# Kernel optimization log

Measured on AMD Instinct MI355X. Metric: run time of the kernel, lower is better.

The kernel has to match this reference:

```python
import jax, jax.numpy as jnp
import numpy as np

N = 100000   # nodes per type (author == paper count here)
E = 800000   # edges per edge type
D = 128      # input feature dim
HID = 128    # hidden_channels
OUT = 64     # out_channels
L = 2        # num_layers


def setup_inputs() -> dict:
    key = jax.random.key(0)
    ks = jax.random.split(key, 14)
    x_author = jax.random.normal(ks[0], (N, D), jnp.float32)
    x_paper = jax.random.normal(ks[1], (N, D), jnp.float32)
    edge_ap = jnp.stack([
        jax.random.randint(ks[2], (E,), 0, N),
        jax.random.randint(ks[3], (E,), 0, N),
    ]).astype(jnp.int32)  # [2,E] author->paper (src,dst)
    # paper->author: ensure every paper id appears as a source so the
    # meta-path conversion keeps all E edges (static shape under jit)
    pa_src = jnp.concatenate([jnp.arange(N), jax.random.randint(ks[4], (E - N,), 0, N)]).astype(jnp.int32)
    pa_dst = jax.random.randint(ks[5], (E,), 0, N).astype(jnp.int32)
    edge_pa = jnp.stack([pa_src, pa_dst])
    perm = jax.random.permutation(ks[6], N).astype(jnp.int32)  # DGI corruption
    s = 0.05
    # SAGEConv params: [layer, edge_type] with edge_type 0 = (author->paper), 1 = (paper->author)
    sage_Wl = jax.random.normal(ks[7], (L, 2, HID, D), jnp.float32) * s   # neighbor lin
    sage_Wr = jax.random.normal(ks[8], (L, 2, HID, D), jnp.float32) * s   # root lin
    sage_b = jnp.zeros((L, 2, HID), jnp.float32)
    # GATConv (heads=1) params
    gat_W = jax.random.normal(ks[9], (OUT, HID), jnp.float32) * s
    gat_att_src = jax.random.normal(ks[10], (OUT,), jnp.float32) * s
    gat_att_dst = jax.random.normal(ks[11], (OUT,), jnp.float32) * s
    gat_b = jnp.zeros((OUT,), jnp.float32)
    prelu_a = jnp.asarray(0.25, jnp.float32)
    return dict(x_author=x_author, x_paper=x_paper, sage_Wl=sage_Wl, sage_Wr=sage_Wr,
                sage_b=sage_b, gat_W=gat_W, gat_att_src=gat_att_src, gat_att_dst=gat_att_dst,
                gat_b=gat_b, prelu_a=prelu_a, edge_ap=edge_ap, edge_pa=edge_pa, perm=perm)


def _sage(x_src, x_dst, src, dst, Wl, Wr, b, n_dst):
    # SAGEConv: mean-aggregate neighbor feats, lin_l(agg) + lin_r(root) + bias
    agg = jax.ops.segment_sum(x_src[src], dst, num_segments=n_dst)       # [n_dst, D]
    cnt = jax.ops.segment_sum(jnp.ones((src.shape[0],), x_src.dtype), dst, num_segments=n_dst)
    mean = agg / jnp.maximum(cnt, 1.0)[:, None]
    return mean @ Wl.T + x_dst @ Wr.T + b


def _gat_prelu(feat, src, dst, W, a_src, a_dst, b, prelu_a, n):
    # GATConv heads=1 (self loops already appended by caller) + PReLU
    h = feat @ W.T                                                        # [n, OUT]
    e = jax.nn.leaky_relu((h @ a_src)[src] + (h @ a_dst)[dst], 0.2)       # [E']
    m = jax.ops.segment_max(e, dst, num_segments=n)
    ex = jnp.exp(e - m[dst])
    den = jax.ops.segment_sum(ex, dst, num_segments=n)
    coef = ex / den[dst]
    out = jax.ops.segment_sum(coef[:, None] * h[src], dst, num_segments=n) + b
    return jnp.where(out >= 0, out, prelu_a * out)


def reference(x_author, x_paper, sage_Wl, sage_Wr, sage_b, gat_W, gat_att_src,
              gat_att_dst, gat_b, prelu_a, edge_ap, edge_pa, perm):
    # Original loop feeds xx_dict into every layer, so only the LAST layer's
    # output survives; and only x_dict['author'] is consumed downstream.
    l = L - 1
    h_author = jax.nn.leaky_relu(
        _sage(x_paper, x_author, edge_pa[0], edge_pa[1],
              sage_Wl[l, 1], sage_Wr[l, 1], sage_b[l, 1], N), 0.01)
    # meta-path author->author edges (paper mapped via last-write paper->author dict)
    p2a = jnp.zeros((N,), jnp.int32).at[edge_pa[0]].set(edge_pa[1])
    self_loop = jnp.arange(N, dtype=jnp.int32)  # GATConv add_self_loops=True
    meta_src = jnp.concatenate([edge_ap[0], self_loop])
    meta_dst = jnp.concatenate([p2a[edge_ap[1]], self_loop])
    pos = _gat_prelu(h_author, meta_src, meta_dst, gat_W, gat_att_src, gat_att_dst, gat_b, prelu_a, N)
    neg = _gat_prelu(h_author[perm], meta_src, meta_dst, gat_W, gat_att_src, gat_att_dst, gat_b, prelu_a, N)
    summary = jnp.mean(pos, axis=0)
    return pos, neg, summary
```

## Files before the change

### kernel.cpp

```cpp
#include <hip/hip_runtime.h>
#include <stdint.h>

#define NN 100000
#define EE 800000
#define DD 128
#define HH 128
#define OO 64

#define SPA 40
#define SME 112

#define PREP_EDGE_B  391
#define PREP_CASTX_B 12500
#define PREP_CASTW_B 40
#define P2_SAGE_B    25000
#define P2_CMP_B     391
#define P3_GEMM_B    782
#define P3_META_B    391

typedef __attribute__((ext_vector_type(8))) short short8v;
typedef __attribute__((ext_vector_type(4))) float f32x4;

__device__ __forceinline__ unsigned short f2bf(float f) {
    union { float f; unsigned int u; } v; v.f = f;
    unsigned int u = v.u;
    u = (u + 0x7fffu + ((u >> 16) & 1u)) >> 16;
    return (unsigned short)u;
}
__device__ __forceinline__ float bf2f(unsigned short b) {
    union { unsigned int u; float f; } v; v.u = ((unsigned int)b) << 16;
    return v.f;
}

__global__ __launch_bounds__(256) void k_prep(const int* __restrict__ pa_src,
                                              const int* __restrict__ pa_dst,
                                              const float* __restrict__ x,
                                              const float* __restrict__ Wl,
                                              const float* __restrict__ Wr,
                                              const float* __restrict__ Wg,
                                              int* __restrict__ amax,
                                              int* __restrict__ cnt_pa,
                                              int* __restrict__ col_pa,
                                              unsigned short* __restrict__ xbf,
                                              unsigned short* __restrict__ wbf) {
    int b = blockIdx.x, t = threadIdx.x;
    if (b < PREP_EDGE_B) {
        int base = (b * 256 + t) * 8;
        if (base + 7 < EE) {
            int4 s0 = *(const int4*)(pa_src + base);
            int4 s1 = *(const int4*)(pa_src + base + 4);
            int4 d0 = *(const int4*)(pa_dst + base);
            int4 d1 = *(const int4*)(pa_dst + base + 4);
            int ss[8] = {s0.x, s0.y, s0.z, s0.w, s1.x, s1.y, s1.z, s1.w};
            int dd[8] = {d0.x, d0.y, d0.z, d0.w, d1.x, d1.y, d1.z, d1.w};
            int pos[8];
            #pragma unroll
            for (int k = 0; k < 8; ++k) atomicMax(&amax[ss[k]], base + k);
            #pragma unroll
            for (int k = 0; k < 8; ++k) pos[k] = atomicAdd(&cnt_pa[dd[k]], 1);
            #pragma unroll
            for (int k = 0; k < 8; ++k)
                if (pos[k] < SPA) __builtin_nontemporal_store(ss[k], &col_pa[dd[k] * SPA + pos[k]]);
        } else {
            for (int e = base; e < EE; ++e) {
                int s = pa_src[e], d = pa_dst[e];
                atomicMax(&amax[s], e);
                int pos = atomicAdd(&cnt_pa[d], 1);
                if (pos < SPA) __builtin_nontemporal_store(s, &col_pa[d * SPA + pos]);
            }
        }
    } else if (b < PREP_EDGE_B + PREP_CASTX_B) {
        long i = (long)(b - PREP_EDGE_B) * 256 + t;
        if (i >= (long)NN * DD / 4) return;
        float4 v = ((const float4*)x)[i];
        ushort4 w;
        w.x = f2bf(v.x); w.y = f2bf(v.y); w.z = f2bf(v.z); w.w = f2bf(v.w);
        ((ushort4*)xbf)[i] = w;
    } else {
        int i4 = (b - PREP_EDGE_B - PREP_CASTX_B) * 256 + t;
        if (i4 >= 10240) return;
        float4 v;
        if (i4 < 4096)       v = ((const float4*)Wl)[i4];
        else if (i4 < 8192)  v = ((const float4*)Wr)[i4 - 4096];
        else                 v = ((const float4*)Wg)[i4 - 8192];
        ushort4 w;
        w.x = f2bf(v.x); w.y = f2bf(v.y); w.z = f2bf(v.z); w.w = f2bf(v.w);
        ((ushort4*)wbf)[i4] = w;
    }
}

__global__ __launch_bounds__(256) void k_pack2(const int* __restrict__ cnt_pa,
                                               const int* __restrict__ col_pa,
                                               const unsigned short* __restrict__ xbf,
                                               const int* __restrict__ amax,
                                               const int* __restrict__ pa_dst,
                                               int* __restrict__ p2a32,
                                               unsigned short* __restrict__ mean_bf) {
    int b = blockIdx.x, t = threadIdx.x;
    if (b < P2_SAGE_B) {
        long gid = (long)b * 256 + t;
        int d = (int)(gid >> 6);
        if (d >= NN) return;
        int lane = (int)(gid & 63);
        int dcnt = cnt_pa[d];
        int deg = (dcnt > SPA) ? SPA : dcnt;
        const int* row = col_pa + d * SPA;
        float ax = 0.f, ay = 0.f;
        int i = 0;
        for (; i + 3 < deg; i += 4) {
            int s0 = row[i], s1 = row[i + 1], s2 = row[i + 2], s3 = row[i + 3];
            ushort2 v0 = ((const ushort2*)(xbf + (long)s0 * DD))[lane];
            ushort2 v1 = ((const ushort2*)(xbf + (long)s1 * DD))[lane];
            ushort2 v2 = ((const ushort2*)(xbf + (long)s2 * DD))[lane];
            ushort2 v3 = ((const ushort2*)(xbf + (long)s3 * DD))[lane];
            ax += (bf2f(v0.x) + bf2f(v1.x)) + (bf2f(v2.x) + bf2f(v3.x));
            ay += (bf2f(v0.y) + bf2f(v1.y)) + (bf2f(v2.y) + bf2f(v3.y));
        }
        for (; i < deg; ++i) {
            int s = row[i];
            ushort2 v = ((const ushort2*)(xbf + (long)s * DD))[lane];
            ax += bf2f(v.x);
            ay += bf2f(v.y);
        }
        float sc = 1.0f / fmaxf((float)dcnt, 1.0f);
        ushort2 w;
        w.x = f2bf(ax * sc);
        w.y = f2bf(ay * sc);
        ((ushort2*)(mean_bf + (long)d * DD))[lane] = w;
    } else {
        int s = (b - P2_SAGE_B) * 256 + t;
        if (s >= NN) return;
        p2a32[s] = pa_dst[amax[s]];
    }
}

__global__ __launch_bounds__(256) void k_pack3(const unsigned short* __restrict__ mean_bf,
                                               const float* __restrict__ xa,
                                               const unsigned short* __restrict__ wbf,
                                               const float* __restrict__ sb,
                                               const float* __restrict__ asrc,
                                               const float* __restrict__ adst,
                                               unsigned short* __restrict__ hg,
                                               float* __restrict__ al_s,
                                               float* __restrict__ al_d,
                                               const int* __restrict__ ap_src,
                                               const int* __restrict__ ap_dst,
                                               const int* __restrict__ p2a32,
                                               int* __restrict__ cnt_meta,
                                               int* __restrict__ col_meta) {
    __shared__ unsigned short hs[4 * 32 * 128];
    int b = blockIdx.x, t = threadIdx.x;
    if (b >= P3_GEMM_B) {
        int base = ((b - P3_GEMM_B) * 256 + t) * 8;
        if (base + 7 < EE) {
            int4 s0 = *(const int4*)(ap_src + base);
            int4 s1 = *(const int4*)(ap_src + base + 4);
            int4 t0 = *(const int4*)(ap_dst + base);
            int4 t1 = *(const int4*)(ap_dst + base + 4);
            int ss[8] = {s0.x, s0.y, s0.z, s0.w, s1.x, s1.y, s1.z, s1.w};
            int tt[8] = {t0.x, t0.y, t0.z, t0.w, t1.x, t1.y, t1.z, t1.w};
            int dd[8], pos[8];
            #pragma unroll
            for (int k = 0; k < 8; ++k) dd[k] = p2a32[tt[k]];
            #pragma unroll
            for (int k = 0; k < 8; ++k) pos[k] = atomicAdd(&cnt_meta[dd[k]], 1);
            #pragma unroll
            for (int k = 0; k < 8; ++k)
                if (pos[k] < SME) __builtin_nontemporal_store(ss[k], &col_meta[dd[k] * SME + pos[k]]);
        } else {
            for (int e = base; e < EE; ++e) {
                int d = p2a32[ap_dst[e]];
                int pos = atomicAdd(&cnt_meta[d], 1);
                if (pos < SME) __builtin_nontemporal_store(ap_src[e], &col_meta[d * SME + pos]);
            }
        }
        return;
    }
    const unsigned short* wl = wbf;
    const unsigned short* wr = wbf + 16384;
    const unsigned short* wg = wbf + 32768;
    int wave = t >> 6, lane = t & 63;
    int rowbase = b * 128 + wave * 32;
    int lr = lane & 15;
    int q = lane >> 4;
    int kq = q * 8;
    int r0 = rowbase + lr, r1 = r0 + 16;
    int cr0 = (r0 < NN) ? r0 : 0;
    int cr1 = (r1 < NN) ? r1 : 0;

    f32x4 acc[2][8];
    #pragma unroll
    for (int i = 0; i < 2; ++i)
        #pragma unroll
        for (int j = 0; j < 8; ++j) { f32x4 z = {0.f,0.f,0.f,0.f}; acc[i][j] = z; }

    #pragma unroll
    for (int k0 = 0; k0 < DD; k0 += 32) {
        int kk = k0 + kq;
        short8v am0 = *(const short8v*)(mean_bf + (long)cr0 * DD + kk);
        short8v am1 = *(const short8v*)(mean_bf + (long)cr1 * DD + kk);
        const float4* q0 = (const float4*)(xa + (long)cr0 * DD + kk);
        const float4* q1 = (const float4*)(xa + (long)cr1 * DD + kk);
        float4 a0 = q0[0], b0 = q0[1], a1 = q1[0], b1 = q1[1];
        short8v ax0, ax1;
        ax0[0]=(short)f2bf(a0.x); ax0[1]=(short)f2bf(a0.y); ax0[2]=(short)f2bf(a0.z); ax0[3]=(short)f2bf(a0.w);
        ax0[4]=(short)f2bf(b0.x); ax0[5]=(short)f2bf(b0.y); ax0[6]=(short)f2bf(b0.z); ax0[7]=(short)f2bf(b0.w);
        ax1[0]=(short)f2bf(a1.x); ax1[1]=(short)f2bf(a1.y); ax1[2]=(short)f2bf(a1.z); ax1[3]=(short)f2bf(a1.w);
        ax1[4]=(short)f2bf(b1.x); ax1[5]=(short)f2bf(b1.y); ax1[6]=(short)f2bf(b1.z); ax1[7]=(short)f2bf(b1.w);
        #pragma unroll
        for (int nb = 0; nb < 8; ++nb) {
            int o = nb * 16 + lr;
            short8v bl = *(const short8v*)(wl + o * DD + kk);
            short8v br = *(const short8v*)(wr + o * DD + kk);
            acc[0][nb] = __builtin_amdgcn_mfma_f32_16x16x32_bf16(am0, bl, acc[0][nb], 0, 0, 0);
            acc[1][nb] = __builtin_amdgcn_mfma_f32_16x16x32_bf16(am1, bl, acc[1][nb], 0, 0, 0);
            acc[0][nb] = __builtin_amdgcn_mfma_f32_16x16x32_bf16(ax0, br, acc[0][nb], 0, 0, 0);
            acc[1][nb] = __builtin_amdgcn_mfma_f32_16x16x32_bf16(ax1, br, acc[1][nb], 0, 0, 0);
        }
    }
    char* hbase = (char*)hs + wave * 8192;
    #pragma unroll
    for (int rh = 0; rh < 2; ++rh) {
        #pragma unroll
        for (int nb = 0; nb < 8; ++nb) {
            int col = nb * 16 + lr;
            float bias = sb[col];
            #pragma unroll
            for (int r = 0; r < 4; ++r) {
                int lrow = rh * 16 + q * 4 + r;
                float v = acc[rh][nb][r] + bias;
                v = (v >= 0.f) ? v : 0.01f * v;
                int boff = (lrow * 256 + col * 2) ^ ((lrow & 7) << 4);
                *(unsigned short*)(hbase + boff) = f2bf(v);
            }
        }
    }
    f32x4 acc2[2][4];
    #pragma unroll
    for (int i = 0; i < 2; ++i)
        #pragma unroll
        for (int j = 0; j < 4; ++j) { f32x4 z = {0.f,0.f,0.f,0.f}; acc2[i][j] = z; }

    #pragma unroll
    for (int k0 = 0; k0 < HH; k0 += 32) {
        int kk = k0 + kq;
        int boff0 = (lr * 256 + kk * 2) ^ ((lr & 7) << 4);
        int boff1 = ((16 + lr) * 256 + kk * 2) ^ ((lr & 7) << 4);
        short8v a0 = *(const short8v*)(hbase + boff0);
        short8v a1 = *(const short8v*)(hbase + boff1);
        #pragma unroll
        for (int nb = 0; nb < 4; ++nb) {
            short8v bg = *(const short8v*)(wg + (nb * 16 + lr) * HH + kk);
            acc2[0][nb] = __builtin_amdgcn_mfma_f32_16x16x32_bf16(a0, bg, acc2[0][nb], 0, 0, 0);
            acc2[1][nb] = __builtin_amdgcn_mfma_f32_16x16x32_bf16(a1, bg, acc2[1][nb], 0, 0, 0);
        }
    }
    float a_s[4], a_d[4];
    #pragma unroll
    for (int nb = 0; nb < 4; ++nb) { a_s[nb] = asrc[nb * 16 + lr]; a_d[nb] = adst[nb * 16 + lr]; }
    #pragma unroll
    for (int rh = 0; rh < 2; ++rh) {
        float ss[4] = {0.f,0.f,0.f,0.f}, dd[4] = {0.f,0.f,0.f,0.f};
        #pragma unroll
        for (int nb = 0; nb < 4; ++nb) {
            #pragma unroll
            for (int r = 0; r < 4; ++r) {
                int row = rowbase + rh * 16 + q * 4 + r;
                unsigned short wb = f2bf(acc2[rh][nb][r]);
                if (row < NN) hg[(long)row * OO + nb * 16 + lr] = wb;
                float w = bf2f(wb);
                ss[r] += w * a_s[nb];
                dd[r] += w * a_d[nb];
            }
        }
        #pragma unroll
        for (int r = 0; r < 4; ++r) {
            float s = ss[r], dv = dd[r];
            #pragma unroll
            for (int off = 1; off < 16; off <<= 1) {
                s  += __shfl_xor(s,  off, 64);
                dv += __shfl_xor(dv, off, 64);
            }
            int row = rowbase + rh * 16 + q * 4 + r;
            if (lr == 0 && row < NN) { al_s[row] = s; al_d[row] = dv; }
        }
    }
}

__global__ __launch_bounds__(256) void k_gat_gather(const int* __restrict__ cnt_meta,
                                                    const int* __restrict__ col_meta,
                                                    const int* __restrict__ perm,
                                                    const float* __restrict__ al_s,
                                                    const float* __restrict__ al_d,
                                                    const unsigned short* __restrict__ hg,
                                                    const float* __restrict__ gb,
                                                    const float* __restrict__ prelu_a,
                                                    float* __restrict__ out) {
    long gid = (long)blockIdx.x * 256 + threadIdx.x;
    int d = (int)(gid >> 6);
    if (d >= NN) return;
    int j = (int)(gid & 63);
    int deg = cnt_meta[d];
    if (deg > SME) deg = SME;
    const int* row = col_meta + d * SME;
    int pd = perm[d];
    float add = al_d[d];
    float adn = al_d[pd];
    float lp = al_s[d] + add;   lp = (lp >= 0.f) ? lp : 0.2f * lp;
    float ln = al_s[pd] + adn;  ln = (ln >= 0.f) ? ln : 0.2f * ln;
    float xps = __expf(lp), xns = __expf(ln);
    float denp = xps, denn = xns;
    float accp = xps * bf2f(hg[((long)d << 6) + j]);
    float accn = xns * bf2f(hg[((long)pd << 6) + j]);

    for (int base = 0; base < deg; base += 64) {
        int cnt = deg - base;
        if (cnt > 64) cnt = 64;
        int s = 0, ps = 0;
        float xp = 0.f, xn = 0.f;
        if (j < cnt) {
            s = row[base + j];
            ps = perm[s];
            float l0 = al_s[s] + add;   l0 = (l0 >= 0.f) ? l0 : 0.2f * l0;
            xp = __expf(l0);
            float m0 = al_s[ps] + adn;  m0 = (m0 >= 0.f) ? m0 : 0.2f * m0;
            xn = __expf(m0);
        }
        float tp = xp, tn = xn;
        #pragma unroll
        for (int off = 32; off; off >>= 1) {
            tp += __shfl_xor(tp, off, 64);
            tn += __shfl_xor(tn, off, 64);
        }
        denp += tp;
        denn += tn;
        int e = 0;
        for (; e + 3 < cnt; e += 4) {
            int s0 = __shfl(s, e),   s1 = __shfl(s, e + 1),   s2 = __shfl(s, e + 2),   s3 = __shfl(s, e + 3);
            int p0 = __shfl(ps, e),  p1 = __shfl(ps, e + 1),  p2 = __shfl(ps, e + 2),  p3 = __shfl(ps, e + 3);
            float a0 = __shfl(xp, e), a1 = __shfl(xp, e + 1), a2 = __shfl(xp, e + 2), a3 = __shfl(xp, e + 3);
            float b0 = __shfl(xn, e), b1 = __shfl(xn, e + 1), b2 = __shfl(xn, e + 2), b3 = __shfl(xn, e + 3);
            float h0 = bf2f(hg[((long)s0 << 6) + j]);
            float h1 = bf2f(hg[((long)s1 << 6) + j]);
            float h2 = bf2f(hg[((long)s2 << 6) + j]);
            float h3 = bf2f(hg[((long)s3 << 6) + j]);
            float g0 = bf2f(hg[((long)p0 << 6) + j]);
            float g1 = bf2f(hg[((long)p1 << 6) + j]);
            float g2 = bf2f(hg[((long)p2 << 6) + j]);
            float g3 = bf2f(hg[((long)p3 << 6) + j]);
            accp += (a0 * h0 + a1 * h1) + (a2 * h2 + a3 * h3);
            accn += (b0 * g0 + b1 * g1) + (b2 * g2 + b3 * g3);
        }
        for (; e < cnt; ++e) {
            int sb2 = __shfl(s, e);
            int pb = __shfl(ps, e);
            float ab = __shfl(xp, e);
            float bb = __shfl(xn, e);
            accp += ab * bf2f(hg[((long)sb2 << 6) + j]);
            accn += bb * bf2f(hg[((long)pb << 6) + j]);
        }
    }
    float bias = gb[j];
    float a = prelu_a[0];
    float vp = accp / denp + bias;
    vp = (vp >= 0.f) ? vp : a * vp;
    out[((long)d << 6) + j] = vp;
    float vn = accn / denn + bias;
    vn = (vn >= 0.f) ? vn : a * vn;
    out[((long)(NN + d) << 6) + j] = vn;
}

__global__ __launch_bounds__(256) void k_summary(const float* __restrict__ out_pos,
                                                 float* __restrict__ summary) {
    int t = threadIdx.x;
    int j = t & 63, sub = t >> 6;
    float acc = 0.f;
    for (int row = blockIdx.x * 4 + sub; row < NN; row += 256 * 4) {
        acc += out_pos[(long)row * OO + j];
    }
    __shared__ float red[4][OO];
    red[sub][j] = acc;
    __syncthreads();
    if (sub == 0) {
        float ttl = red[0][j] + red[1][j] + red[2][j] + red[3][j];
        atomicAdd(summary + j, ttl * (1.0f / NN));
    }
}

extern "C" void kernel_launch(void* const* d_in, const int* in_sizes, int n_in,
                              void* d_out, int out_size, void* d_ws, size_t ws_size,
                              hipStream_t stream) {
    const float* x_author = (const float*)d_in[0];
    const float* x_paper  = (const float*)d_in[1];
    const float* sage_Wl  = (const float*)d_in[2];
    const float* sage_Wr  = (const float*)d_in[3];
    const float* sage_b   = (const float*)d_in[4];
    const float* gat_W    = (const float*)d_in[5];
    const float* gat_as   = (const float*)d_in[6];
    const float* gat_ad   = (const float*)d_in[7];
    const float* gat_b    = (const float*)d_in[8];
    const float* prelu_a  = (const float*)d_in[9];
    const int*   edge_ap  = (const int*)d_in[10];
    const int*   edge_pa  = (const int*)d_in[11];
    const int*   perm     = (const int*)d_in[12];

    char* ws = (char*)d_ws;
    int*   cnt_pa    = (int*)(ws + 0);
    int*   cnt_meta  = (int*)(ws + 400000);
    int*   amax      = (int*)(ws + 800000);
    int*   p2a32     = (int*)(ws + 1200000);
    float* al_s      = (float*)(ws + 1600000);
    float* al_d      = (float*)(ws + 2000000);
    unsigned short* wbf = (unsigned short*)(ws + 2400000);
    int*   col_pa    = (int*)(ws + 2481920);
    unsigned short* mean_bf = (unsigned short*)(ws + 18481920);
    unsigned short* xbf     = (unsigned short*)(ws + 44081920);
    int*   col_meta  = (int*)(ws + 44081920);
    unsigned short* hg = (unsigned short*)col_pa;

    hipMemsetAsync(d_ws, 0, 1200000, stream);
    hipMemsetAsync((char*)d_out + (size_t)2 * NN * OO * sizeof(float), 0,
                   OO * sizeof(float), stream);

    const float* Wl = sage_Wl + 3 * HH * DD;
    const float* Wr = sage_Wr + 3 * HH * DD;
    const float* sb = sage_b  + 3 * HH;

    k_prep<<<PREP_EDGE_B + PREP_CASTX_B + PREP_CASTW_B, 256, 0, stream>>>(
        edge_pa, edge_pa + EE, x_paper, Wl, Wr, gat_W, amax, cnt_pa, col_pa, xbf, wbf);
    k_pack2<<<P2_SAGE_B + P2_CMP_B, 256, 0, stream>>>(
        cnt_pa, col_pa, xbf, amax, edge_pa + EE, p2a32, mean_bf);
    k_pack3<<<P3_GEMM_B + P3_META_B, 256, 0, stream>>>(
        mean_bf, x_author, wbf, sb, gat_as, gat_ad, hg, al_s, al_d,
        edge_ap, edge_ap + EE, p2a32, cnt_meta, col_meta);
    k_gat_gather<<<(NN * 64 + 255) / 256, 256, 0, stream>>>(cnt_meta, col_meta, perm,
                                                            al_s, al_d, hg, gat_b, prelu_a,
                                                            (float*)d_out);
    k_summary<<<256, 256, 0, stream>>>((float*)d_out, (float*)d_out + 2L * NN * OO);
}
```

Before: 337.2 us.

## Bucket edges by destination block then build CSR rows in shared memory

Replaces direct per-node atomic scatter into global adjacency rows with a two-pass scheme. Edges are first bucketed into 1024 coarse buckets of 98 destination nodes (packed local-dst<<17|src); per-bucket blocks then build fixed-width adjacency rows in LDS and write them out coalesced. This applies to both the SAGE paper->author graph and the meta-path graph, and also folds the p2a lookup into the meta scatter. It aims to cut scattered global atomics and random writes, at the cost of an extra kernel launch, extra passes over the edge data, and fixed bucket capacities that could silently drop edges on skewed inputs.

```diff
diff --git a/kernel.cpp b/kernel.cpp
--- a/kernel.cpp
+++ b/kernel.cpp
@@ -9,14 +9,17 @@
 
 #define SPA 40
 #define SME 112
+#define NB  1024
+#define BA  98
+#define CAPA 1024
+#define CAPM 2048
 
 #define PREP_EDGE_B  391
 #define PREP_CASTX_B 12500
 #define PREP_CASTW_B 40
-#define P2_SAGE_B    25000
-#define P2_CMP_B     391
-#define P3_GEMM_B    782
-#define P3_META_B    391
+#define SCATM_B      391
+#define SAGE_B       25000
+#define GEMM_B       782
 
 typedef __attribute__((ext_vector_type(8))) short short8v;
 typedef __attribute__((ext_vector_type(4))) float f32x4;
@@ -39,8 +42,8 @@
                                               const float* __restrict__ Wr,
                                               const float* __restrict__ Wg,
                                               int* __restrict__ amax,
-                                              int* __restrict__ cnt_pa,
-                                              int* __restrict__ col_pa,
+                                              int* __restrict__ curA,
+                                              int* __restrict__ sortedA,
                                               unsigned short* __restrict__ xbf,
                                               unsigned short* __restrict__ wbf) {
     int b = blockIdx.x, t = threadIdx.x;
@@ -53,20 +56,25 @@
             int4 d1 = *(const int4*)(pa_dst + base + 4);
             int ss[8] = {s0.x, s0.y, s0.z, s0.w, s1.x, s1.y, s1.z, s1.w};
             int dd[8] = {d0.x, d0.y, d0.z, d0.w, d1.x, d1.y, d1.z, d1.w};
-            int pos[8];
             #pragma unroll
             for (int k = 0; k < 8; ++k) atomicMax(&amax[ss[k]], base + k);
             #pragma unroll
-            for (int k = 0; k < 8; ++k) pos[k] = atomicAdd(&cnt_pa[dd[k]], 1);
-            #pragma unroll
-            for (int k = 0; k < 8; ++k)
-                if (pos[k] < SPA) __builtin_nontemporal_store(ss[k], &col_pa[dd[k] * SPA + pos[k]]);
+            for (int k = 0; k < 8; ++k) {
+                int bk = dd[k] / BA;
+                int pos = atomicAdd(&curA[bk], 1);
+                if (pos < CAPA)
+                    __builtin_nontemporal_store(((dd[k] - bk * BA) << 17) | ss[k],
+                                                &sortedA[bk * CAPA + pos]);
+            }
         } else {
             for (int e = base; e < EE; ++e) {
                 int s = pa_src[e], d = pa_dst[e];
                 atomicMax(&amax[s], e);
-                int pos = atomicAdd(&cnt_pa[d], 1);
-                if (pos < SPA) __builtin_nontemporal_store(s, &col_pa[d * SPA + pos]);
+                int bk = d / BA;
+                int pos = atomicAdd(&curA[bk], 1);
+                if (pos < CAPA)
+                    __builtin_nontemporal_store(((d - bk * BA) << 17) | s,
+                                                &sortedA[bk * CAPA + pos]);
             }
         }
     } else if (b < PREP_EDGE_B + PREP_CASTX_B) {
@@ -89,52 +97,93 @@
     }
 }
 
-__global__ __launch_bounds__(256) void k_pack2(const int* __restrict__ cnt_pa,
-                                               const int* __restrict__ col_pa,
-                                               const unsigned short* __restrict__ xbf,
+__global__ __launch_bounds__(256) void k_pack2(const int* __restrict__ ap_src,
+                                               const int* __restrict__ ap_dst,
                                                const int* __restrict__ amax,
                                                const int* __restrict__ pa_dst,
-                                               int* __restrict__ p2a32,
-                                               unsigned short* __restrict__ mean_bf) {
+                                               int* __restrict__ curM,
+                                               int* __restrict__ sortedM,
+                                               const int* __restrict__ curA,
+                                               const int* __restrict__ sortedA,
+                                               int* __restrict__ cnt_pa,
+                                               int* __restrict__ col_pa) {
+    __shared__ int cntA[BA];
+    __shared__ int colA[BA * SPA];
     int b = blockIdx.x, t = threadIdx.x;
-    if (b < P2_SAGE_B) {
-        long gid = (long)b * 256 + t;
-        int d = (int)(gid >> 6);
-        if (d >= NN) return;
-        int lane = (int)(gid & 63);
-        int dcnt = cnt_pa[d];
-        int deg = (dcnt > SPA) ? SPA : dcnt;
-        const int* row = col_pa + d * SPA;
-        float ax = 0.f, ay = 0.f;
-        int i = 0;
-        for (; i + 3 < deg; i += 4) {
-            int s0 = row[i], s1 = row[i + 1], s2 = row[i + 2], s3 = row[i + 3];
-            ushort2 v0 = ((const ushort2*)(xbf + (long)s0 * DD))[lane];
-            ushort2 v1 = ((const ushort2*)(xbf + (long)s1 * DD))[lane];
-            ushort2 v2 = ((const ushort2*)(xbf + (long)s2 * DD))[lane];
-            ushort2 v3 = ((const ushort2*)(xbf + (long)s3 * DD))[lane];
-            ax += (bf2f(v0.x) + bf2f(v1.x)) + (bf2f(v2.x) + bf2f(v3.x));
-            ay += (bf2f(v0.y) + bf2f(v1.y)) + (bf2f(v2.y) + bf2f(v3.y));
-        }
-        for (; i < deg; ++i) {
-            int s = row[i];
-            ushort2 v = ((const ushort2*)(xbf + (long)s * DD))[lane];
-            ax += bf2f(v.x);
-            ay += bf2f(v.y);
-        }
-        float sc = 1.0f / fmaxf((float)dcnt, 1.0f);
-        ushort2 w;
-        w.x = f2bf(ax * sc);
-        w.y = f2bf(ay * sc);
-        ((ushort2*)(mean_bf + (long)d * DD))[lane] = w;
-    } else {
-        int s = (b - P2_SAGE_B) * 256 + t;
-        if (s >= NN) return;
-        p2a32[s] = pa_dst[amax[s]];
-    }
-}
-
-__global__ __launch_bounds__(256) void k_pack3(const unsigned short* __restrict__ mean_bf,
+    if (b < SCATM_B) {
+        int base = (b * 256 + t) * 8;
+        #pragma unroll
+        for (int k = 0; k < 8; ++k) {
+            int e = base + k;
+            if (e < EE) {
+                int p = ap_dst[e];
+                int d = pa_dst[amax[p]];
+                int bk = d / BA;
+                int pos = atomicAdd(&curM[bk], 1);
+                if (pos < CAPM)
+                    __builtin_nontemporal_store(((d - bk * BA) << 17) | ap_src[e],
+                                                &sortedM[bk * CAPM + pos]);
+            }
+        }
+        return;
+    }
+    int bk = b - SCATM_B;
+    if (t < BA) cntA[t] = 0;
+    __syncthreads();
+    int n = curA[bk];
+    if (n > CAPA) n = CAPA;
+    const int* src = sortedA + bk * CAPA;
+    for (int i = t; i < n; i += 256) {
+        int w = src[i];
+        int dl = w >> 17, s = w & 0x1ffff;
+        int pos = atomicAdd(&cntA[dl], 1);
+        if (pos < SPA) colA[dl * SPA + pos] = s;
+    }
+    __syncthreads();
+    long gbase = (long)bk * BA;
+    if (t < BA && gbase + t < NN) cnt_pa[gbase + t] = cntA[t];
+    long cbase = gbase * SPA;
+    for (int i = t; i < BA * SPA; i += 256) {
+        if (gbase + i / SPA < NN) col_pa[cbase + i] = colA[i];
+    }
+}
+
+__global__ __launch_bounds__(256) void k_sage(const int* __restrict__ cnt_pa,
+                                              const int* __restrict__ col_pa,
+                                              const unsigned short* __restrict__ xbf,
+                                              unsigned short* __restrict__ mean_bf) {
+    long gid = (long)blockIdx.x * 256 + threadIdx.x;
+    int d = (int)(gid >> 6);
+    if (d >= NN) return;
+    int lane = (int)(gid & 63);
+    int dcnt = cnt_pa[d];
+    int deg = (dcnt > SPA) ? SPA : dcnt;
+    const int* row = col_pa + d * SPA;
+    float ax = 0.f, ay = 0.f;
+    int i = 0;
+    for (; i + 3 < deg; i += 4) {
+        int s0 = row[i], s1 = row[i + 1], s2 = row[i + 2], s3 = row[i + 3];
+        ushort2 v0 = ((const ushort2*)(xbf + (long)s0 * DD))[lane];
+        ushort2 v1 = ((const ushort2*)(xbf + (long)s1 * DD))[lane];
+        ushort2 v2 = ((const ushort2*)(xbf + (long)s2 * DD))[lane];
+        ushort2 v3 = ((const ushort2*)(xbf + (long)s3 * DD))[lane];
+        ax += (bf2f(v0.x) + bf2f(v1.x)) + (bf2f(v2.x) + bf2f(v3.x));
+        ay += (bf2f(v0.y) + bf2f(v1.y)) + (bf2f(v2.y) + bf2f(v3.y));
+    }
+    for (; i < deg; ++i) {
+        int s = row[i];
+        ushort2 v = ((const ushort2*)(xbf + (long)s * DD))[lane];
+        ax += bf2f(v.x);
+        ay += bf2f(v.y);
+    }
+    float sc = 1.0f / fmaxf((float)dcnt, 1.0f);
+    ushort2 w;
+    w.x = f2bf(ax * sc);
+    w.y = f2bf(ay * sc);
+    ((ushort2*)(mean_bf + (long)d * DD))[lane] = w;
+}
+
+__global__ __launch_bounds__(256) void k_pack4(const unsigned short* __restrict__ mean_bf,
                                                const float* __restrict__ xa,
                                                const unsigned short* __restrict__ wbf,
                                                const float* __restrict__ sb,
@@ -143,39 +192,37 @@
                                                unsigned short* __restrict__ hg,
                                                float* __restrict__ al_s,
                                                float* __restrict__ al_d,
-                                               const int* __restrict__ ap_src,
-                                               const int* __restrict__ ap_dst,
-                                               const int* __restrict__ p2a32,
+                                               const int* __restrict__ curM,
+                                               const int* __restrict__ sortedM,
                                                int* __restrict__ cnt_meta,
                                                int* __restrict__ col_meta) {
-    __shared__ unsigned short hs[4 * 32 * 128];
+    __shared__ int smem[11200];
     int b = blockIdx.x, t = threadIdx.x;
-    if (b >= P3_GEMM_B) {
-        int base = ((b - P3_GEMM_B) * 256 + t) * 8;
-        if (base + 7 < EE) {
-            int4 s0 = *(const int4*)(ap_src + base);
-            int4 s1 = *(const int4*)(ap_src + base + 4);
-            int4 t0 = *(const int4*)(ap_dst + base);
-            int4 t1 = *(const int4*)(ap_dst + base + 4);
-            int ss[8] = {s0.x, s0.y, s0.z, s0.w, s1.x, s1.y, s1.z, s1.w};
-            int tt[8] = {t0.x, t0.y, t0.z, t0.w, t1.x, t1.y, t1.z, t1.w};
-            int dd[8], pos[8];
-            #pragma unroll
-            for (int k = 0; k < 8; ++k) dd[k] = p2a32[tt[k]];
-            #pragma unroll
-            for (int k = 0; k < 8; ++k) pos[k] = atomicAdd(&cnt_meta[dd[k]], 1);
-            #pragma unroll
-            for (int k = 0; k < 8; ++k)
-                if (pos[k] < SME) __builtin_nontemporal_store(ss[k], &col_meta[dd[k] * SME + pos[k]]);
-        } else {
-            for (int e = base; e < EE; ++e) {
-                int d = p2a32[ap_dst[e]];
-                int pos = atomicAdd(&cnt_meta[d], 1);
-                if (pos < SME) __builtin_nontemporal_store(ap_src[e], &col_meta[d * SME + pos]);
-            }
+    if (b >= GEMM_B) {
+        int bk = b - GEMM_B;
+        int* cntM = smem;
+        int* colM = smem + BA;
+        if (t < BA) cntM[t] = 0;
+        __syncthreads();
+        int n = curM[bk];
+        if (n > CAPM) n = CAPM;
+        const int* src = sortedM + bk * CAPM;
+        for (int i = t; i < n; i += 256) {
+            int w = src[i];
+            int dl = w >> 17, s = w & 0x1ffff;
+            int pos = atomicAdd(&cntM[dl], 1);
+            if (pos < SME) colM[dl * SME + pos] = s;
+        }
+        __syncthreads();
+        long gbase = (long)bk * BA;
+        if (t < BA && gbase + t < NN) cnt_meta[gbase + t] = cntM[t];
+        long cbase = gbase * SME;
+        for (int i = t; i < BA * SME; i += 256) {
+            if (gbase + i / SME < NN) col_meta[cbase + i] = colM[i];
         }
         return;
     }
+    unsigned short* hs = (unsigned short*)smem;
     const unsigned short* wl = wbf;
     const unsigned short* wr = wbf + 16384;
     const unsigned short* wg = wbf + 32768;
@@ -302,7 +349,7 @@
     int j = (int)(gid & 63);
     int deg = cnt_meta[d];
     if (deg > SME) deg = SME;
-    const int* row = col_meta + d * SME;
+    const int* row = col_meta + (long)d * SME;
     int pd = perm[d];
     float add = al_d[d];
     float adn = al_d[pd];
@@ -405,20 +452,23 @@
     const int*   perm     = (const int*)d_in[12];
 
     char* ws = (char*)d_ws;
-    int*   cnt_pa    = (int*)(ws + 0);
-    int*   cnt_meta  = (int*)(ws + 400000);
-    int*   amax      = (int*)(ws + 800000);
-    int*   p2a32     = (int*)(ws + 1200000);
-    float* al_s      = (float*)(ws + 1600000);
-    float* al_d      = (float*)(ws + 2000000);
-    unsigned short* wbf = (unsigned short*)(ws + 2400000);
-    int*   col_pa    = (int*)(ws + 2481920);
-    unsigned short* mean_bf = (unsigned short*)(ws + 18481920);
-    unsigned short* xbf     = (unsigned short*)(ws + 44081920);
-    int*   col_meta  = (int*)(ws + 44081920);
+    int*   amax      = (int*)(ws + 0);
+    int*   curA      = (int*)(ws + 400000);
+    int*   curM      = (int*)(ws + 404096);
+    float* al_s      = (float*)(ws + 408192);
+    float* al_d      = (float*)(ws + 808192);
+    unsigned short* wbf = (unsigned short*)(ws + 1208192);
+    int*   cnt_pa    = (int*)(ws + 1290112);
+    int*   cnt_meta  = (int*)(ws + 1690112);
+    int*   sortedA   = (int*)(ws + 2090112);
+    int*   sortedM   = (int*)(ws + 6284416);
+    int*   col_pa    = (int*)(ws + 14673024);
+    unsigned short* xbf = (unsigned short*)(ws + 30673024);
+    int*   col_meta  = (int*)(ws + 30673024);
+    unsigned short* mean_bf = (unsigned short*)(ws + 75473024);
     unsigned short* hg = (unsigned short*)col_pa;
 
-    hipMemsetAsync(d_ws, 0, 1200000, stream);
+    hipMemsetAsync(d_ws, 0, 408192, stream);
     hipMemsetAsync((char*)d_out + (size_t)2 * NN * OO * sizeof(float), 0,
                    OO * sizeof(float), stream);
 
@@ -427,12 +477,14 @@
     const float* sb = sage_b  + 3 * HH;
 
     k_prep<<<PREP_EDGE_B + PREP_CASTX_B + PREP_CASTW_B, 256, 0, stream>>>(
-        edge_pa, edge_pa + EE, x_paper, Wl, Wr, gat_W, amax, cnt_pa, col_pa, xbf, wbf);
-    k_pack2<<<P2_SAGE_B + P2_CMP_B, 256, 0, stream>>>(
-        cnt_pa, col_pa, xbf, amax, edge_pa + EE, p2a32, mean_bf);
-    k_pack3<<<P3_GEMM_B + P3_META_B, 256, 0, stream>>>(
+        edge_pa, edge_pa + EE, x_paper, Wl, Wr, gat_W, amax, curA, sortedA, xbf, wbf);
+    k_pack2<<<SCATM_B + NB, 256, 0, stream>>>(
+        edge_ap, edge_ap + EE, amax, edge_pa + EE, curM, sortedM,
+        curA, sortedA, cnt_pa, col_pa);
+    k_sage<<<SAGE_B, 256, 0, stream>>>(cnt_pa, col_pa, xbf, mean_bf);
+    k_pack4<<<GEMM_B + NB, 256, 0, stream>>>(
         mean_bf, x_author, wbf, sb, gat_as, gat_ad, hg, al_s, al_d,
-        edge_ap, edge_ap + EE, p2a32, cnt_meta, col_meta);
+        curM, sortedM, cnt_meta, col_meta);
     k_gat_gather<<<(NN * 64 + 255) / 256, 256, 0, stream>>>(cnt_meta, col_meta, perm,
                                                             al_s, al_d, hg, gat_b, prelu_a,
                                                             (float*)d_out);
```

Measured after the change: 567.5 us. 1.68x slower.
